# Performance work log

Hardware: AMD Instinct MI355X
Metric: run time of the kernel (lower is better)

The kernel has to match this reference:

```python
import jax, jax.numpy as jnp
import numpy as np

LAMBDA = 0.1


def setup_inputs() -> dict:
    key = jax.random.key(0)
    k1, k2 = jax.random.split(key)
    shape = (32, 1, 1024, 1024)  # [B, C, H, W], H/W power of 2 (required by the quadtree recursion)
    D_est = jax.random.uniform(k1, shape, dtype=jnp.float32)
    D_gt = jax.random.uniform(k2, shape, dtype=jnp.float32)
    return {"D_est": D_est, "D_gt": D_gt}


def reference(D_est, D_gt):
    # recursive_search bottoms out at 1x1 regions; crowd_count sums over ALL
    # dims (batch/channel included), so for power-of-2 spatial dims the mask
    # is exactly a per-pixel comparison of batch+channel-summed counts,
    # broadcast back over batch/channel.
    s_est = jnp.sum(D_est, axis=(0, 1))  # [H, W]
    s_gt = jnp.sum(D_gt, axis=(0, 1))    # [H, W]
    mask = (s_est > s_gt).astype(D_est.dtype)  # broadcasts over [B, C, H, W]

    diff2 = jnp.sum(jnp.square(D_est - D_gt))          # ||D_est - D_gt||^2
    G2 = jnp.sum(jnp.square(D_est))                    # ||G||^2
    H2 = jnp.sum(jnp.square(D_est * mask))             # ||H||^2
    return diff2 / G2 + LAMBDA * (diff2 / H2)
```

## Files before the change

kernel.cpp:

```cpp
#include <hip/hip_runtime.h>

constexpr int B       = 32;
constexpr int HW      = 1024 * 1024;
constexpr int NP4     = HW / 4;
constexpr int CHUNK   = 8;
constexpr int THREADS = 256;
constexpr int GRID    = NP4 / THREADS;

typedef float floatx4 __attribute__((ext_vector_type(4)));

__device__ __forceinline__ floatx4 nt_load(const floatx4* p) {
    return __builtin_nontemporal_load(p);
}

__global__ __launch_bounds__(THREADS, 4) void pra_main_kernel(
    const float* __restrict__ est,
    const float* __restrict__ gt,
    double* __restrict__ acc)
{
    const int t = blockIdx.x * blockDim.x + threadIdx.x;
    const floatx4* e_ptr = reinterpret_cast<const floatx4*>(est) + t;
    const floatx4* g_ptr = reinterpret_cast<const floatx4*>(gt) + t;

    floatx4 dse = {0.f, 0.f, 0.f, 0.f};
    floatx4 q   = {0.f, 0.f, 0.f, 0.f};
    float   d2  = 0.f;

    #pragma unroll
    for (int c = 0; c < B; c += CHUNK) {
        floatx4 eb[CHUNK], gb[CHUNK];
        #pragma unroll
        for (int j = 0; j < CHUNK; ++j)
            eb[j] = nt_load(e_ptr + (size_t)(c + j) * NP4);
        #pragma unroll
        for (int j = 0; j < CHUNK; ++j)
            gb[j] = nt_load(g_ptr + (size_t)(c + j) * NP4);
        #pragma unroll
        for (int j = 0; j < CHUNK; ++j) {
            floatx4 e = eb[j], g = gb[j];
            floatx4 d = e - g;
            dse += d;
            q   += e * e;
            floatx4 dd = d * d;
            d2 += dd.x + dd.y + dd.z + dd.w;
        }
    }

    float g2 = q.x + q.y + q.z + q.w;
    float h2 = (dse.x > 0.f ? q.x : 0.f) + (dse.y > 0.f ? q.y : 0.f) +
               (dse.z > 0.f ? q.z : 0.f) + (dse.w > 0.f ? q.w : 0.f);

    #pragma unroll
    for (int off = 32; off > 0; off >>= 1) {
        d2 += __shfl_down(d2, off);
        g2 += __shfl_down(g2, off);
        h2 += __shfl_down(h2, off);
    }

    __shared__ float sd[4], sG[4], sH[4];
    const int wave = threadIdx.x >> 6;
    const int lane = threadIdx.x & 63;
    if (lane == 0) { sd[wave] = d2; sG[wave] = g2; sH[wave] = h2; }
    __syncthreads();
    if (threadIdx.x == 0) {
        float D = sd[0] + sd[1] + sd[2] + sd[3];
        float G = sG[0] + sG[1] + sG[2] + sG[3];
        float H = sH[0] + sH[1] + sH[2] + sH[3];
        atomicAdd(&acc[0], (double)D);
        atomicAdd(&acc[1], (double)G);
        atomicAdd(&acc[2], (double)H);
    }
}

__global__ void pra_final_kernel(const double* __restrict__ acc,
                                 float* __restrict__ out)
{
    if (threadIdx.x == 0 && blockIdx.x == 0) {
        double d2 = acc[0], g2 = acc[1], h2 = acc[2];
        out[0] = (float)(d2 / g2 + 0.1 * (d2 / h2));
    }
}

extern "C" void kernel_launch(void* const* d_in, const int* in_sizes, int n_in,
                              void* d_out, int out_size, void* d_ws, size_t ws_size,
                              hipStream_t stream)
{
    const float* d_est = (const float*)d_in[0];
    const float* d_gt  = (const float*)d_in[1];
    float* out = (float*)d_out;
    double* acc = (double*)d_ws;

    pra_main_kernel<<<GRID, THREADS, 0, stream>>>(d_est, d_gt, acc);
    pra_final_kernel<<<1, 64, 0, stream>>>(acc, out);
}
```

Baseline: 267.6 us.

## Split batch reduction across two thread teams per pixel block

```diff
diff --git a/kernel.cpp b/kernel.cpp
--- a/kernel.cpp
+++ b/kernel.cpp
@@ -1,11 +1,13 @@
 #include <hip/hip_runtime.h>
 
 constexpr int B       = 32;
+constexpr int HB      = B / 2;
 constexpr int HW      = 1024 * 1024;
 constexpr int NP4     = HW / 4;
-constexpr int CHUNK   = 8;
-constexpr int THREADS = 256;
-constexpr int GRID    = NP4 / THREADS;
+constexpr int CHUNK   = 4;
+constexpr int THREADS = 512;
+constexpr int PIXB    = 256;
+constexpr int GRID    = NP4 / PIXB;
 
 typedef float floatx4 __attribute__((ext_vector_type(4)));
 
@@ -13,21 +15,24 @@
     return __builtin_nontemporal_load(p);
 }
 
-__global__ __launch_bounds__(THREADS, 4) void pra_main_kernel(
+__global__ __launch_bounds__(THREADS, 8) void pra_main_kernel(
     const float* __restrict__ est,
     const float* __restrict__ gt,
     double* __restrict__ acc)
 {
-    const int t = blockIdx.x * blockDim.x + threadIdx.x;
-    const floatx4* e_ptr = reinterpret_cast<const floatx4*>(est) + t;
-    const floatx4* g_ptr = reinterpret_cast<const floatx4*>(gt) + t;
+    const int team = threadIdx.x >> 8;
+    const int r    = threadIdx.x & 255;
+    const int pix4 = blockIdx.x * PIXB + r;
+    const size_t boff = (size_t)team * HB * NP4;
+    const floatx4* e_ptr = reinterpret_cast<const floatx4*>(est) + boff + pix4;
+    const floatx4* g_ptr = reinterpret_cast<const floatx4*>(gt) + boff + pix4;
 
     floatx4 dse = {0.f, 0.f, 0.f, 0.f};
     floatx4 q   = {0.f, 0.f, 0.f, 0.f};
     float   d2  = 0.f;
 
     #pragma unroll
-    for (int c = 0; c < B; c += CHUNK) {
+    for (int c = 0; c < HB; c += CHUNK) {
         floatx4 eb[CHUNK], gb[CHUNK];
         #pragma unroll
         for (int j = 0; j < CHUNK; ++j)
@@ -46,9 +51,19 @@
         }
     }
 
-    float g2 = q.x + q.y + q.z + q.w;
-    float h2 = (dse.x > 0.f ? q.x : 0.f) + (dse.y > 0.f ? q.y : 0.f) +
-               (dse.z > 0.f ? q.z : 0.f) + (dse.w > 0.f ? q.w : 0.f);
+    __shared__ floatx4 s_dse[PIXB];
+    __shared__ floatx4 s_q[PIXB];
+    if (team == 1) { s_dse[r] = dse; s_q[r] = q; }
+    __syncthreads();
+
+    float g2 = 0.f, h2 = 0.f;
+    if (team == 0) {
+        floatx4 dt = dse + s_dse[r];
+        floatx4 qt = q   + s_q[r];
+        g2 = qt.x + qt.y + qt.z + qt.w;
+        h2 = (dt.x > 0.f ? qt.x : 0.f) + (dt.y > 0.f ? qt.y : 0.f) +
+             (dt.z > 0.f ? qt.z : 0.f) + (dt.w > 0.f ? qt.w : 0.f);
+    }
 
     #pragma unroll
     for (int off = 32; off > 0; off >>= 1) {
@@ -57,15 +72,15 @@
         h2 += __shfl_down(h2, off);
     }
 
-    __shared__ float sd[4], sG[4], sH[4];
+    __shared__ float sd[8], sG[8], sH[8];
     const int wave = threadIdx.x >> 6;
     const int lane = threadIdx.x & 63;
     if (lane == 0) { sd[wave] = d2; sG[wave] = g2; sH[wave] = h2; }
     __syncthreads();
     if (threadIdx.x == 0) {
-        float D = sd[0] + sd[1] + sd[2] + sd[3];
-        float G = sG[0] + sG[1] + sG[2] + sG[3];
-        float H = sH[0] + sH[1] + sH[2] + sH[3];
+        float D = 0.f, G = 0.f, H = 0.f;
+        #pragma unroll
+        for (int w = 0; w < 8; ++w) { D += sd[w]; G += sG[w]; H += sH[w]; }
         atomicAdd(&acc[0], (double)D);
         atomicAdd(&acc[1], (double)G);
         atomicAdd(&acc[2], (double)H);
```

Result: slower. 295.3 us (+10.4%).

## Process four pixel-quads per thread with two-batch load bursts and sched barrier

Applied to the files above, without the earlier changes.

```diff
diff --git a/kernel.cpp b/kernel.cpp
--- a/kernel.cpp
+++ b/kernel.cpp
@@ -3,9 +3,11 @@
 constexpr int B       = 32;
 constexpr int HW      = 1024 * 1024;
 constexpr int NP4     = HW / 4;
-constexpr int CHUNK   = 8;
+constexpr int P       = 4;
 constexpr int THREADS = 256;
-constexpr int GRID    = NP4 / THREADS;
+constexpr int BLOCK_PIX4 = THREADS * P;
+constexpr int GRID    = NP4 / BLOCK_PIX4;
+constexpr int BURST   = 2;
 
 typedef float floatx4 __attribute__((ext_vector_type(4)));
 
@@ -18,37 +20,52 @@
     const float* __restrict__ gt,
     double* __restrict__ acc)
 {
-    const int t = blockIdx.x * blockDim.x + threadIdx.x;
-    const floatx4* e_ptr = reinterpret_cast<const floatx4*>(est) + t;
-    const floatx4* g_ptr = reinterpret_cast<const floatx4*>(gt) + t;
+    const int base = blockIdx.x * BLOCK_PIX4 + threadIdx.x;
+    const floatx4* e0 = reinterpret_cast<const floatx4*>(est) + base;
+    const floatx4* g0 = reinterpret_cast<const floatx4*>(gt) + base;
 
-    floatx4 dse = {0.f, 0.f, 0.f, 0.f};
-    floatx4 q   = {0.f, 0.f, 0.f, 0.f};
-    float   d2  = 0.f;
+    floatx4 dse[P] = {{0.f,0.f,0.f,0.f},{0.f,0.f,0.f,0.f},
+                      {0.f,0.f,0.f,0.f},{0.f,0.f,0.f,0.f}};
+    floatx4 q[P]   = {{0.f,0.f,0.f,0.f},{0.f,0.f,0.f,0.f},
+                      {0.f,0.f,0.f,0.f},{0.f,0.f,0.f,0.f}};
+    float d2 = 0.f;
 
     #pragma unroll
-    for (int c = 0; c < B; c += CHUNK) {
-        floatx4 eb[CHUNK], gb[CHUNK];
+    for (int b = 0; b < B; b += BURST) {
+        floatx4 eb[BURST][P], gb[BURST][P];
         #pragma unroll
-        for (int j = 0; j < CHUNK; ++j)
-            eb[j] = nt_load(e_ptr + (size_t)(c + j) * NP4);
+        for (int s = 0; s < BURST; ++s)
+            #pragma unroll
+            for (int k = 0; k < P; ++k)
+                eb[s][k] = nt_load(e0 + (size_t)(b + s) * NP4 + k * THREADS);
         #pragma unroll
-        for (int j = 0; j < CHUNK; ++j)
-            gb[j] = nt_load(g_ptr + (size_t)(c + j) * NP4);
+        for (int s = 0; s < BURST; ++s)
+            #pragma unroll
+            for (int k = 0; k < P; ++k)
+                gb[s][k] = nt_load(g0 + (size_t)(b + s) * NP4 + k * THREADS);
+        __builtin_amdgcn_sched_barrier(0);
+
         #pragma unroll
-        for (int j = 0; j < CHUNK; ++j) {
-            floatx4 e = eb[j], g = gb[j];
-            floatx4 d = e - g;
-            dse += d;
-            q   += e * e;
-            floatx4 dd = d * d;
-            d2 += dd.x + dd.y + dd.z + dd.w;
+        for (int s = 0; s < BURST; ++s) {
+            #pragma unroll
+            for (int k = 0; k < P; ++k) {
+                floatx4 e = eb[s][k], g = gb[s][k];
+                floatx4 d = e - g;
+                dse[k] += d;
+                q[k]   += e * e;
+                floatx4 dd = d * d;
+                d2 += dd.x + dd.y + dd.z + dd.w;
+            }
         }
     }
 
-    float g2 = q.x + q.y + q.z + q.w;
-    float h2 = (dse.x > 0.f ? q.x : 0.f) + (dse.y > 0.f ? q.y : 0.f) +
-               (dse.z > 0.f ? q.z : 0.f) + (dse.w > 0.f ? q.w : 0.f);
+    float g2 = 0.f, h2 = 0.f;
+    #pragma unroll
+    for (int k = 0; k < P; ++k) {
+        g2 += q[k].x + q[k].y + q[k].z + q[k].w;
+        h2 += (dse[k].x > 0.f ? q[k].x : 0.f) + (dse[k].y > 0.f ? q[k].y : 0.f) +
+              (dse[k].z > 0.f ? q[k].z : 0.f) + (dse[k].w > 0.f ? q[k].w : 0.f);
+    }
 
     #pragma unroll
     for (int off = 32; off > 0; off >>= 1) {
```

Measured after the change: 249.8 us. -6.6%, faster.
